# Kernel tuning notes

Hardware: AMD Instinct MI355X
Metric: run time of the kernel (lower is better)

The kernel has to match this reference:

```python
import jax, jax.numpy as jnp
import numpy as np

NEG_SLOPE = 0.1

def leaky(x):
    return jnp.where(x >= 0, x, NEG_SLOPE * x)

def setup_inputs() -> dict:
    key = jax.random.key(0)
    ks = jax.random.split(key, 9)
    B, N, K, Cin, Cout = 4, 16384, 16, 64, 128
    xyz = jax.random.normal(ks[0], (B, 3, N), jnp.float32)
    features = jax.random.normal(ks[1], (B, Cin, N), jnp.float32)
    knn_indices = jax.random.randint(ks[2], (B, N, K), 0, N)
    # weight_net: MLP2d(3, [8,16]) == two 1x1 convs with leaky_relu
    w1 = jax.random.normal(ks[3], (8, 3), jnp.float32) * 0.3
    b1 = jax.random.normal(ks[4], (8,), jnp.float32) * 0.05
    w2 = jax.random.normal(ks[5], (16, 8), jnp.float32) * 0.2
    b2 = jax.random.normal(ks[6], (16,), jnp.float32) * 0.05
    lin_w = jax.random.normal(ks[7], (Cout, 16 * (Cin + 3)), jnp.float32) * 0.02
    lin_b = jax.random.normal(ks[8], (Cout,), jnp.float32) * 0.02
    return {"xyz": xyz, "features": features, "knn_indices": knn_indices,
            "w1": w1, "b1": b1, "w2": w2, "b2": b2,
            "lin_w": lin_w, "lin_b": lin_b}

def reference(xyz, features, knn_indices, w1, b1, w2, b2, lin_w, lin_b):
    B, _, N = xyz.shape
    K = knn_indices.shape[2]
    # channel-last views
    xyz_cl = xyz.transpose(0, 2, 1)                                  # [B,N,3]
    feats_cl = jnp.concatenate([xyz, features], axis=1).transpose(0, 2, 1)  # [B,N,3+C]
    gather = jax.vmap(lambda f, i: f[i])                             # per-batch gather
    knn_xyz = gather(xyz_cl, knn_indices)                            # [B,N,K,3]
    knn_xyz_norm = knn_xyz - xyz_cl[:, :, None, :]                   # [B,N,K,3]
    # weight_net (1x1 conv MLP: 3 -> 8 -> 16, leaky_relu)
    h = leaky(jnp.einsum('bnkc,oc->bnko', knn_xyz_norm, w1) + b1)    # [B,N,K,8]
    w = leaky(jnp.einsum('bnkh,oh->bnko', h, w2) + b2)               # [B,N,K,16]
    knn_feats = gather(feats_cl, knn_indices)                        # [B,N,K,3+C]
    # weights^T @ knn_features, flattened (16, 3+C) -> 16*(3+C)
    agg = jnp.einsum('bnkw,bnkc->bnwc', w, knn_feats).reshape(B, N, -1)
    out = leaky(agg @ lin_w.T + lin_b)                               # [B,N,Cout]
    return out.transpose(0, 2, 1)                                    # [B,Cout,N]
```

## Files before the change

### kernel.cpp

```cpp
#include <hip/hip_runtime.h>
#include <hip/hip_bf16.h>

#define B_    4
#define N_    16384
#define K_    16
#define CIN_  64
#define CF_   67
#define COUT_ 128
#define AGGP_ 1088
#define P_    32
#define PH_   16
#define FSTR  64
#define ASTR  1096
#define WTS   272
#define NEG_  0.1f

typedef __attribute__((ext_vector_type(8))) short short8;
typedef __attribute__((ext_vector_type(4))) float f32x4;
typedef __attribute__((ext_vector_type(2))) unsigned int uint2_t;
typedef __attribute__((ext_vector_type(4))) unsigned int uint4_t;

__device__ __forceinline__ unsigned short f2b(float f) {
    __hip_bfloat16 h = __float2bfloat16(f);
    return *reinterpret_cast<unsigned short*>(&h);
}
__device__ __forceinline__ float leaky(float x) { return x >= 0.f ? x : NEG_ * x; }

__global__ __launch_bounds__(256) void pc_prep(
    const float* __restrict__ xyz,
    const float* __restrict__ feats,
    const float* __restrict__ lin_w,
    unsigned short* __restrict__ ft,
    short* __restrict__ lwb,
    float* __restrict__ xyz3)
{
    const int bid = blockIdx.x, t = threadIdx.x;
    if (bid < 1024) {
        __shared__ float st[64][69];
        const int b  = bid >> 8;
        const int j0 = (bid & 255) << 6;
        for (int ii = t; ii < 68 * 16; ii += 256) {
            const int c = ii >> 4, jq = ii & 15;
            f32x4 v = {0.f, 0.f, 0.f, 0.f};
            if (c < 3)
                v = *(const f32x4*)(xyz   + ((size_t)b * 3    + c)       * N_ + j0 + 4 * jq);
            else if (c < CF_)
                v = *(const f32x4*)(feats + ((size_t)b * CIN_ + (c - 3)) * N_ + j0 + 4 * jq);
            st[4 * jq + 0][c] = v.x;
            st[4 * jq + 1][c] = v.y;
            st[4 * jq + 2][c] = v.z;
            st[4 * jq + 3][c] = v.w;
        }
        __syncthreads();
        if (t < 64) {
            f32x4 v = { st[t][0], st[t][1], st[t][2], 0.f };
            *(f32x4*)(xyz3 + ((size_t)(b * N_ + j0 + t)) * 4) = v;
        }
        uint4_t* outp4 = (uint4_t*)(ft + (size_t)(b * N_ + j0) * FSTR);
        for (int idx = t; idx < 64 * 8; idx += 256) {
            const int j2 = idx >> 3, q = idx & 7;
            const int cb = 3 + q * 8;
            unsigned u[4];
#pragma unroll
            for (int e = 0; e < 4; e++) {
                const int c0 = cb + 2 * e;
                u[e] = (unsigned)f2b(st[j2][c0]) | ((unsigned)f2b(st[j2][c0 + 1]) << 16);
            }
            uint4_t uu = { u[0], u[1], u[2], u[3] };
            outp4[idx] = uu;
        }
    } else {
        const int o = bid - 1024;
        const float* src = lin_w + (size_t)o * (16 * CF_);
        short*       dst = lwb   + (size_t)o * AGGP_;
        for (int i = t; i < AGGP_; i += 256) {
            const int w = i / 68, c = i % 68;
            const int sc = (c < 64) ? (3 + c) : (c - 64);
            dst[i] = (c < CF_) ? (short)f2b(src[w * CF_ + sc]) : (short)0;
        }
    }
}

__device__ __forceinline__ void gather_ft(const unsigned short* ftb, const int* ip,
                                          int s, uint2_t* fb)
{
#pragma unroll
    for (int k = 0; k < K_; k++) {
        const unsigned short* rec = ftb + (size_t)ip[k] * FSTR;
        fb[k] = *(const uint2_t*)(rec + 4 * s);
    }
}

__device__ __forceinline__ void mlp_store(
    short* wd, float d0, float d1, float d2,
    const float* w1, const float* b1, const float* w2, const float* b2)
{
    float hh[8];
#pragma unroll
    for (int i = 0; i < 8; i++)
        hh[i] = leaky(b1[i] + w1[i*3+0]*d0 + w1[i*3+1]*d1 + w1[i*3+2]*d2);
#pragma unroll
    for (int w = 0; w < 16; w++) {
        float a = b2[w];
#pragma unroll
        for (int i = 0; i < 8; i++) a += w2[w*8+i] * hh[i];
        wd[w * 16] = (short)f2b(leaky(a));
    }
}

__device__ __forceinline__ void transpose_store(
    short* frow, const uint2_t* fb, int s)
{
    const int hf = ((s >> 2) & 1) << 3;
#pragma unroll
    for (int i = 0; i < 4; i++) {
        const unsigned sel = (i & 1) ? 0x07060302u : 0x05040100u;
        unsigned pk[8];
#pragma unroll
        for (int d = 0; d < 8; d++) {
            const unsigned lo = (i < 2) ? fb[2*d].x   : fb[2*d].y;
            const unsigned hi = (i < 2) ? fb[2*d+1].x : fb[2*d+1].y;
            pk[d] = __builtin_amdgcn_perm(hi, lo, sel);
        }
        const int c   = 4 * s + i;
        const int row = c ^ (s & 3);
        uint4_t q0 = { pk[0], pk[1], pk[2], pk[3] };
        uint4_t q1 = { pk[4], pk[5], pk[6], pk[7] };
        *(uint4_t*)(frow + row * 16 + hf)       = q0;
        *(uint4_t*)(frow + row * 16 + (8 - hf)) = q1;
    }
    if (s == 3) {
        uint4_t z = {0u, 0u, 0u, 0u};
        *(uint4_t*)(frow + 67 * 16)     = z;
        *(uint4_t*)(frow + 67 * 16 + 8) = z;
    }
}

__device__ __forceinline__ void agg_mfma(short* s_aggp, const short* s_WTp,
                                         int t, int pbase)
{
    const int lane = t & 63;
    const int wq   = lane >> 4;
    const int pr   = lane & 15;
    const int pbl  = (t >> 6) * 4;
    const int kh   = (wq & 1) * 8;
    const int side = (wq < 2) ? 0 : 1;
    const int asid = (pr < 8) ? 0 : 1;
    const bool act = (side == asid);
    const int cq   = 4 * (wq & 1);
    const int c0   = pr & 7;
    const int bb   = c0 >> 2;
#pragma unroll
    for (int pair = 0; pair < 2; pair++) {
        const int lpA = pbl + 2 * pair;
        const int ppA = pbase + lpA;
        const short8 bfr = *(const short8*)(s_WTp + (lpA + side) * WTS + pr * 16 + kh);
        const short* ap  = s_aggp + (size_t)(ppA + asid) * ASTR;
        f32x4 D[9];
#pragma unroll
        for (int cc = 0; cc < 9; cc++) {
            const int row  = (c0 + 8 * cc) ^ ((bb + 2 * cc) & 3);
            const int khcc = kh ^ (((cc >> 1) & 1) << 3);
            short8 af = {0,0,0,0,0,0,0,0};
            if (act && (cc < 8 || c0 < 4))
                af = *(const short8*)(ap + row * 16 + khcc);
            D[cc] = __builtin_amdgcn_mfma_f32_16x16x32_bf16(
                        af, bfr, (f32x4){0.f,0.f,0.f,0.f}, 0, 0, 0);
        }
        __asm__ __volatile__("" ::: "memory");
        short* arow = s_aggp + (size_t)(ppA + side) * ASTR + pr * 68;
#pragma unroll
        for (int cc = 0; cc < 9; cc++) {
            if (cc == 8 && cq != 0) continue;
            const unsigned lo = (unsigned)f2b(D[cc].x) | ((unsigned)f2b(D[cc].y) << 16);
            const unsigned hi = (unsigned)f2b(D[cc].z) | ((unsigned)f2b(D[cc].w) << 16);
            uint2_t pk2 = { lo, hi };
            *(uint2_t*)(arow + 8 * cc + cq) = pk2;
        }
    }
}

__global__ __launch_bounds__(256, 2) void pc_main(
    const float*          __restrict__ x3,
    const unsigned short* __restrict__ ft,
    const int*            __restrict__ knn,
    const float* __restrict__ w1, const float* __restrict__ b1,
    const float* __restrict__ w2, const float* __restrict__ b2,
    const short* __restrict__ lwb, const float* __restrict__ lin_b,
    float* __restrict__ out)
{
    __shared__ __align__(16) short s_agg[P_ * ASTR];
    __shared__ __align__(16) short s_WT[PH_ * WTS];
    __shared__ int s_idx[2 * PH_ * K_];

    const int t   = threadIdx.x;
    const int bid = blockIdx.x;
    const int b   = bid >> 9;
    const int n0  = (bid & 511) << 5;
    const unsigned short* ftb = ft + (size_t)b * N_ * FSTR;
    const f32x4* x3b = (const f32x4*)x3 + (size_t)b * N_;

    const int p = t >> 4, s = t & 15;

    const int n_a = n0 + p, n_b = n0 + PH_ + p;
    const int ja = knn[((size_t)(b * N_ + n_a)) * K_ + s];
    const int jb = knn[((size_t)(b * N_ + n_b)) * K_ + s];
    s_idx[(0 * PH_ + p) * K_ + s] = ja;
    s_idx[(1 * PH_ + p) * K_ + s] = jb;
    const f32x4 qa = x3b[ja], qb = x3b[jb];
    const f32x4 ca = x3b[n_a], cb = x3b[n_b];
    const float dxa0 = qa.x - ca.x, dxa1 = qa.y - ca.y, dxa2 = qa.z - ca.z;
    const float dxb0 = qb.x - cb.x, dxb1 = qb.y - cb.y, dxb2 = qb.z - cb.z;
    __asm__ __volatile__("" ::: "memory");

    const int* ipa = s_idx + (0 * PH_ + p) * K_;
    const int* ipb = s_idx + (1 * PH_ + p) * K_;
    uint2_t fbA[K_], fbB[K_];
    gather_ft(ftb, ipa, s, fbA);
    gather_ft(ftb, ipb, s, fbB);

    {
        short* frow = s_agg + (size_t)p * ASTR;
        frow[64 * 16 + s] = (short)f2b(qa.x);
        frow[65 * 16 + s] = (short)f2b(qa.y);
        frow[66 * 16 + s] = (short)f2b(qa.z);
    }
    mlp_store(s_WT + p * WTS + s, dxa0, dxa1, dxa2, w1, b1, w2, b2);
    __asm__ __volatile__("" ::: "memory");
    transpose_store(s_agg + (size_t)p * ASTR, fbA, s);
    __asm__ __volatile__("" ::: "memory");
    agg_mfma(s_agg, s_WT, t, 0);
    __asm__ __volatile__("" ::: "memory");

    {
        short* frow = s_agg + (size_t)(PH_ + p) * ASTR;
        frow[64 * 16 + s] = (short)f2b(qb.x);
        frow[65 * 16 + s] = (short)f2b(qb.y);
        frow[66 * 16 + s] = (short)f2b(qb.z);
    }
    mlp_store(s_WT + p * WTS + s, dxb0, dxb1, dxb2, w1, b1, w2, b2);
    __asm__ __volatile__("" ::: "memory");
    transpose_store(s_agg + (size_t)(PH_ + p) * ASTR, fbB, s);
    __asm__ __volatile__("" ::: "memory");
    agg_mfma(s_agg, s_WT, t, PH_);

    {
        const int lane = t & 63, wid = t >> 6;
        const int quad = lane >> 4, pr = lane & 15;
        const int kq = quad * 8;
        const short* a0p = lwb + (size_t)(wid * 32 + pr) * AGGP_ + kq;
        const short* a1p = a0p + 16 * AGGP_;

        short8 pa0[6], pa1[6];
#pragma unroll
        for (int d = 0; d < 6; d++) {
            pa0[d] = *(const short8*)(a0p + 32 * d);
            pa1[d] = *(const short8*)(a1p + 32 * d);
        }
        __syncthreads();

        const short* bp0 = s_agg + (size_t)pr * ASTR + kq;
        const short* bp1 = s_agg + (size_t)(16 + pr) * ASTR + kq;
        f32x4 acc00 = {0.f, 0.f, 0.f, 0.f};
        f32x4 acc01 = {0.f, 0.f, 0.f, 0.f};
        f32x4 acc10 = {0.f, 0.f, 0.f, 0.f};
        f32x4 acc11 = {0.f, 0.f, 0.f, 0.f};

#pragma unroll
        for (int ks = 0; ks < 34; ks++) {
            const int d = ks % 6;
            const short8 a0c = pa0[d], a1c = pa1[d];
            if (ks + 6 < 34) {
                pa0[d] = *(const short8*)(a0p + 32 * (ks + 6));
                pa1[d] = *(const short8*)(a1p + 32 * (ks + 6));
            }
            const short8 b0 = *(const short8*)(bp0 + 32 * ks);
            const short8 b1 = *(const short8*)(bp1 + 32 * ks);
            acc00 = __builtin_amdgcn_mfma_f32_16x16x32_bf16(a0c, b0, acc00, 0, 0, 0);
            acc01 = __builtin_amdgcn_mfma_f32_16x16x32_bf16(a0c, b1, acc01, 0, 0, 0);
            acc10 = __builtin_amdgcn_mfma_f32_16x16x32_bf16(a1c, b0, acc10, 0, 0, 0);
            acc11 = __builtin_amdgcn_mfma_f32_16x16x32_bf16(a1c, b1, acc11, 0, 0, 0);
        }
        const int o0 = wid * 32 + quad * 4;
#pragma unroll
        for (int r = 0; r < 4; r++) {
            const int oA = o0 + r;
            const int oB = oA + 16;
            const float bA = lin_b[oA], bB = lin_b[oB];
            float* rowA = out + ((size_t)(b * COUT_ + oA)) * N_ + n0;
            float* rowB = out + ((size_t)(b * COUT_ + oB)) * N_ + n0;
            rowA[pr]      = leaky(acc00[r] + bA);
            rowA[16 + pr] = leaky(acc01[r] + bA);
            rowB[pr]      = leaky(acc10[r] + bB);
            rowB[16 + pr] = leaky(acc11[r] + bB);
        }
    }
}

extern "C" void kernel_launch(void* const* d_in, const int* in_sizes, int n_in,
                              void* d_out, int out_size, void* d_ws, size_t ws_size,
                              hipStream_t stream)
{
    const float* xyz   = (const float*)d_in[0];
    const float* feats = (const float*)d_in[1];
    const int*   knn   = (const int*)d_in[2];
    const float* w1    = (const float*)d_in[3];
    const float* b1    = (const float*)d_in[4];
    const float* w2    = (const float*)d_in[5];
    const float* b2    = (const float*)d_in[6];
    const float* lin_w = (const float*)d_in[7];
    const float* lin_b = (const float*)d_in[8];
    float* out = (float*)d_out;

    const size_t ftBytes  = (size_t)B_ * N_ * FSTR * sizeof(short);
    const size_t lwbBytes = (size_t)COUT_ * AGGP_ * sizeof(short);
    unsigned short* ft   = (unsigned short*)d_ws;
    short*          lwb  = (short*)((char*)d_ws + ftBytes);
    float*          xyz3 = (float*)((char*)d_ws + ftBytes + lwbBytes);

    hipLaunchKernelGGL(pc_prep, dim3(1024 + COUT_), dim3(256), 0, stream,
                       xyz, feats, lin_w, ft, lwb, xyz3);
    hipLaunchKernelGGL(pc_main, dim3(B_ * (N_ / P_)), dim3(256), 0, stream,
                       xyz3, ft, knn, w1, b1, w2, b2, lwb, lin_b, out);
}
```

Measured before the change: 183.3 us.

## Double threads per block to split gather, MLP, and output GEMM work

```diff
diff --git a/kernel.cpp b/kernel.cpp
--- a/kernel.cpp
+++ b/kernel.cpp
@@ -82,17 +82,17 @@
 }
 
 __device__ __forceinline__ void gather_ft(const unsigned short* ftb, const int* ip,
-                                          int s, uint2_t* fb)
+                                          int s5, unsigned* fb)
 {
 #pragma unroll
     for (int k = 0; k < K_; k++) {
         const unsigned short* rec = ftb + (size_t)ip[k] * FSTR;
-        fb[k] = *(const uint2_t*)(rec + 4 * s);
+        fb[k] = *(const unsigned*)(rec + 2 * s5);
     }
 }
 
 __device__ __forceinline__ void mlp_store(
-    short* wd, float d0, float d1, float d2,
+    short* wd, int wh, float d0, float d1, float d2,
     const float* w1, const float* b1, const float* w2, const float* b2)
 {
     float hh[8];
@@ -100,7 +100,8 @@
     for (int i = 0; i < 8; i++)
         hh[i] = leaky(b1[i] + w1[i*3+0]*d0 + w1[i*3+1]*d1 + w1[i*3+2]*d2);
 #pragma unroll
-    for (int w = 0; w < 16; w++) {
+    for (int j = 0; j < 8; j++) {
+        const int w = wh * 8 + j;
         float a = b2[w];
 #pragma unroll
         for (int i = 0; i < 8; i++) a += w2[w*8+i] * hh[i];
@@ -109,27 +110,24 @@
 }
 
 __device__ __forceinline__ void transpose_store(
-    short* frow, const uint2_t* fb, int s)
-{
-    const int hf = ((s >> 2) & 1) << 3;
-#pragma unroll
-    for (int i = 0; i < 4; i++) {
+    short* frow, const unsigned* fb, int s5)
+{
+#pragma unroll
+    for (int i = 0; i < 2; i++) {
         const unsigned sel = (i & 1) ? 0x07060302u : 0x05040100u;
         unsigned pk[8];
 #pragma unroll
-        for (int d = 0; d < 8; d++) {
-            const unsigned lo = (i < 2) ? fb[2*d].x   : fb[2*d].y;
-            const unsigned hi = (i < 2) ? fb[2*d+1].x : fb[2*d+1].y;
-            pk[d] = __builtin_amdgcn_perm(hi, lo, sel);
-        }
-        const int c   = 4 * s + i;
-        const int row = c ^ (s & 3);
+        for (int d = 0; d < 8; d++)
+            pk[d] = __builtin_amdgcn_perm(fb[2*d+1], fb[2*d], sel);
+        const int c   = 2 * s5 + i;
+        const int row = c ^ ((c >> 2) & 3);
+        const int hf  = ((c >> 4) & 1) << 3;
         uint4_t q0 = { pk[0], pk[1], pk[2], pk[3] };
         uint4_t q1 = { pk[4], pk[5], pk[6], pk[7] };
         *(uint4_t*)(frow + row * 16 + hf)       = q0;
         *(uint4_t*)(frow + row * 16 + (8 - hf)) = q1;
     }
-    if (s == 3) {
+    if (s5 == 3) {
         uint4_t z = {0u, 0u, 0u, 0u};
         *(uint4_t*)(frow + 67 * 16)     = z;
         *(uint4_t*)(frow + 67 * 16 + 8) = z;
@@ -142,7 +140,7 @@
     const int lane = t & 63;
     const int wq   = lane >> 4;
     const int pr   = lane & 15;
-    const int pbl  = (t >> 6) * 4;
+    const int pbl  = (t >> 6) * 2;
     const int kh   = (wq & 1) * 8;
     const int side = (wq < 2) ? 0 : 1;
     const int asid = (pr < 8) ? 0 : 1;
@@ -150,37 +148,33 @@
     const int cq   = 4 * (wq & 1);
     const int c0   = pr & 7;
     const int bb   = c0 >> 2;
-#pragma unroll
-    for (int pair = 0; pair < 2; pair++) {
-        const int lpA = pbl + 2 * pair;
-        const int ppA = pbase + lpA;
-        const short8 bfr = *(const short8*)(s_WTp + (lpA + side) * WTS + pr * 16 + kh);
-        const short* ap  = s_aggp + (size_t)(ppA + asid) * ASTR;
-        f32x4 D[9];
-#pragma unroll
-        for (int cc = 0; cc < 9; cc++) {
-            const int row  = (c0 + 8 * cc) ^ ((bb + 2 * cc) & 3);
-            const int khcc = kh ^ (((cc >> 1) & 1) << 3);
-            short8 af = {0,0,0,0,0,0,0,0};
-            if (act && (cc < 8 || c0 < 4))
-                af = *(const short8*)(ap + row * 16 + khcc);
-            D[cc] = __builtin_amdgcn_mfma_f32_16x16x32_bf16(
-                        af, bfr, (f32x4){0.f,0.f,0.f,0.f}, 0, 0, 0);
-        }
-        __asm__ __volatile__("" ::: "memory");
-        short* arow = s_aggp + (size_t)(ppA + side) * ASTR + pr * 68;
-#pragma unroll
-        for (int cc = 0; cc < 9; cc++) {
-            if (cc == 8 && cq != 0) continue;
-            const unsigned lo = (unsigned)f2b(D[cc].x) | ((unsigned)f2b(D[cc].y) << 16);
-            const unsigned hi = (unsigned)f2b(D[cc].z) | ((unsigned)f2b(D[cc].w) << 16);
-            uint2_t pk2 = { lo, hi };
-            *(uint2_t*)(arow + 8 * cc + cq) = pk2;
-        }
-    }
-}
-
-__global__ __launch_bounds__(256, 2) void pc_main(
+    const int ppA  = pbase + pbl;
+    const short8 bfr = *(const short8*)(s_WTp + (pbl + side) * WTS + pr * 16 + kh);
+    const short* ap  = s_aggp + (size_t)(ppA + asid) * ASTR;
+    f32x4 D[9];
+#pragma unroll
+    for (int cc = 0; cc < 9; cc++) {
+        const int row  = (c0 + 8 * cc) ^ ((bb + 2 * cc) & 3);
+        const int khcc = kh ^ (((cc >> 1) & 1) << 3);
+        short8 af = {0,0,0,0,0,0,0,0};
+        if (act && (cc < 8 || c0 < 4))
+            af = *(const short8*)(ap + row * 16 + khcc);
+        D[cc] = __builtin_amdgcn_mfma_f32_16x16x32_bf16(
+                    af, bfr, (f32x4){0.f,0.f,0.f,0.f}, 0, 0, 0);
+    }
+    __asm__ __volatile__("" ::: "memory");
+    short* arow = s_aggp + (size_t)(ppA + side) * ASTR + pr * 68;
+#pragma unroll
+    for (int cc = 0; cc < 9; cc++) {
+        if (cc == 8 && cq != 0) continue;
+        const unsigned lo = (unsigned)f2b(D[cc].x) | ((unsigned)f2b(D[cc].y) << 16);
+        const unsigned hi = (unsigned)f2b(D[cc].z) | ((unsigned)f2b(D[cc].w) << 16);
+        uint2_t pk2 = { lo, hi };
+        *(uint2_t*)(arow + 8 * cc + cq) = pk2;
+    }
+}
+
+__global__ __launch_bounds__(512, 4) void pc_main(
     const float*          __restrict__ x3,
     const unsigned short* __restrict__ ft,
     const int*            __restrict__ knn,
@@ -200,13 +194,18 @@
     const unsigned short* ftb = ft + (size_t)b * N_ * FSTR;
     const f32x4* x3b = (const f32x4*)x3 + (size_t)b * N_;
 
-    const int p = t >> 4, s = t & 15;
+    const int p  = t >> 5;
+    const int s5 = t & 31;
+    const int k  = s5 & 15;
+    const int wh = s5 >> 4;
 
     const int n_a = n0 + p, n_b = n0 + PH_ + p;
-    const int ja = knn[((size_t)(b * N_ + n_a)) * K_ + s];
-    const int jb = knn[((size_t)(b * N_ + n_b)) * K_ + s];
-    s_idx[(0 * PH_ + p) * K_ + s] = ja;
-    s_idx[(1 * PH_ + p) * K_ + s] = jb;
+    const int ja = knn[((size_t)(b * N_ + n_a)) * K_ + k];
+    const int jb = knn[((size_t)(b * N_ + n_b)) * K_ + k];
+    if (wh == 0) {
+        s_idx[(0 * PH_ + p) * K_ + k] = ja;
+        s_idx[(1 * PH_ + p) * K_ + k] = jb;
+    }
     const f32x4 qa = x3b[ja], qb = x3b[jb];
     const f32x4 ca = x3b[n_a], cb = x3b[n_b];
     const float dxa0 = qa.x - ca.x, dxa1 = qa.y - ca.y, dxa2 = qa.z - ca.z;
@@ -215,32 +214,32 @@
 
     const int* ipa = s_idx + (0 * PH_ + p) * K_;
     const int* ipb = s_idx + (1 * PH_ + p) * K_;
-    uint2_t fbA[K_], fbB[K_];
-    gather_ft(ftb, ipa, s, fbA);
-    gather_ft(ftb, ipb, s, fbB);
-
-    {
+    unsigned fbA[K_], fbB[K_];
+    gather_ft(ftb, ipa, s5, fbA);
+    gather_ft(ftb, ipb, s5, fbB);
+
+    if (wh == 0) {
         short* frow = s_agg + (size_t)p * ASTR;
-        frow[64 * 16 + s] = (short)f2b(qa.x);
-        frow[65 * 16 + s] = (short)f2b(qa.y);
-        frow[66 * 16 + s] = (short)f2b(qa.z);
-    }
-    mlp_store(s_WT + p * WTS + s, dxa0, dxa1, dxa2, w1, b1, w2, b2);
-    __asm__ __volatile__("" ::: "memory");
-    transpose_store(s_agg + (size_t)p * ASTR, fbA, s);
+        frow[64 * 16 + k] = (short)f2b(qa.x);
+        frow[65 * 16 + k] = (short)f2b(qa.y);
+        frow[66 * 16 + k] = (short)f2b(qa.z);
+    }
+    mlp_store(s_WT + p * WTS + k, wh, dxa0, dxa1, dxa2, w1, b1, w2, b2);
+    __asm__ __volatile__("" ::: "memory");
+    transpose_store(s_agg + (size_t)p * ASTR, fbA, s5);
     __asm__ __volatile__("" ::: "memory");
     agg_mfma(s_agg, s_WT, t, 0);
     __asm__ __volatile__("" ::: "memory");
 
-    {
+    if (wh == 0) {
         short* frow = s_agg + (size_t)(PH_ + p) * ASTR;
-        frow[64 * 16 + s] = (short)f2b(qb.x);
-        frow[65 * 16 + s] = (short)f2b(qb.y);
-        frow[66 * 16 + s] = (short)f2b(qb.z);
-    }
-    mlp_store(s_WT + p * WTS + s, dxb0, dxb1, dxb2, w1, b1, w2, b2);
-    __asm__ __volatile__("" ::: "memory");
-    transpose_store(s_agg + (size_t)(PH_ + p) * ASTR, fbB, s);
+        frow[64 * 16 + k] = (short)f2b(qb.x);
+        frow[65 * 16 + k] = (short)f2b(qb.y);
+        frow[66 * 16 + k] = (short)f2b(qb.z);
+    }
+    mlp_store(s_WT + p * WTS + k, wh, dxb0, dxb1, dxb2, w1, b1, w2, b2);
+    __asm__ __volatile__("" ::: "memory");
+    transpose_store(s_agg + (size_t)(PH_ + p) * ASTR, fbB, s5);
     __asm__ __volatile__("" ::: "memory");
     agg_mfma(s_agg, s_WT, t, PH_);
 
@@ -248,51 +247,38 @@
         const int lane = t & 63, wid = t >> 6;
         const int quad = lane >> 4, pr = lane & 15;
         const int kq = quad * 8;
-        const short* a0p = lwb + (size_t)(wid * 32 + pr) * AGGP_ + kq;
-        const short* a1p = a0p + 16 * AGGP_;
-
-        short8 pa0[6], pa1[6];
-#pragma unroll
-        for (int d = 0; d < 6; d++) {
+        const short* a0p = lwb + (size_t)(wid * 16 + pr) * AGGP_ + kq;
+
+        short8 pa0[6];
+#pragma unroll
+        for (int d = 0; d < 6; d++)
             pa0[d] = *(const short8*)(a0p + 32 * d);
-            pa1[d] = *(const short8*)(a1p + 32 * d);
-        }
         __syncthreads();
 
         const short* bp0 = s_agg + (size_t)pr * ASTR + kq;
         const short* bp1 = s_agg + (size_t)(16 + pr) * ASTR + kq;
         f32x4 acc00 = {0.f, 0.f, 0.f, 0.f};
         f32x4 acc01 = {0.f, 0.f, 0.f, 0.f};
-        f32x4 acc10 = {0.f, 0.f, 0.f, 0.f};
-        f32x4 acc11 = {0.f, 0.f, 0.f, 0.f};
 
 #pragma unroll
         for (int ks = 0; ks < 34; ks++) {
             const int d = ks % 6;
-            const short8 a0c = pa0[d], a1c = pa1[d];
-            if (ks + 6 < 34) {
+            const short8 a0c = pa0[d];
+            if (ks + 6 < 34)
                 pa0[d] = *(const short8*)(a0p + 32 * (ks + 6));
-                pa1[d] = *(const short8*)(a1p + 32 * (ks + 6));
-            }
             const short8 b0 = *(const short8*)(bp0 + 32 * ks);
             const short8 b1 = *(const short8*)(bp1 + 32 * ks);
             acc00 = __builtin_amdgcn_mfma_f32_16x16x32_bf16(a0c, b0, acc00, 0, 0, 0);
             acc01 = __builtin_amdgcn_mfma_f32_16x16x32_bf16(a0c, b1, acc01, 0, 0, 0);
-            acc10 = __builtin_amdgcn_mfma_f32_16x16x32_bf16(a1c, b0, acc10, 0, 0, 0);
-            acc11 = __builtin_amdgcn_mfma_f32_16x16x32_bf16(a1c, b1, acc11, 0, 0, 0);
-        }
-        const int o0 = wid * 32 + quad * 4;
+        }
+        const int o0 = wid * 16 + quad * 4;
 #pragma unroll
         for (int r = 0; r < 4; r++) {
             const int oA = o0 + r;
-            const int oB = oA + 16;
-            const float bA = lin_b[oA], bB = lin_b[oB];
+            const float bA = lin_b[oA];
             float* rowA = out + ((size_t)(b * COUT_ + oA)) * N_ + n0;
-            float* rowB = out + ((size_t)(b * COUT_ + oB)) * N_ + n0;
             rowA[pr]      = leaky(acc00[r] + bA);
             rowA[16 + pr] = leaky(acc01[r] + bA);
-            rowB[pr]      = leaky(acc10[r] + bB);
-            rowB[16 + pr] = leaky(acc11[r] + bB);
         }
     }
 }
@@ -320,6 +306,6 @@
 
     hipLaunchKernelGGL(pc_prep, dim3(1024 + COUT_), dim3(256), 0, stream,
                        xyz, feats, lin_w, ft, lwb, xyz3);
-    hipLaunchKernelGGL(pc_main, dim3(B_ * (N_ / P_)), dim3(256), 0, stream,
+    hipLaunchKernelGGL(pc_main, dim3(B_ * (N_ / P_)), dim3(512), 0, stream,
                        xyz3, ft, knn, w1, b1, w2, b2, lwb, lin_b, out);
 }
```

After: 202.7 us. 10.6% more time.

## Halve points per block to 16 and raise occupancy to three blocks per CU

Applied to the files above, without the earlier changes.

```diff
diff --git a/kernel.cpp b/kernel.cpp
--- a/kernel.cpp
+++ b/kernel.cpp
@@ -8,8 +8,7 @@
 #define CF_   67
 #define COUT_ 128
 #define AGGP_ 1088
-#define P_    32
-#define PH_   16
+#define P_    16
 #define FSTR  64
 #define ASTR  1096
 #define WTS   272
@@ -136,8 +135,7 @@
     }
 }
 
-__device__ __forceinline__ void agg_mfma(short* s_aggp, const short* s_WTp,
-                                         int t, int pbase)
+__device__ __forceinline__ void agg_mfma(short* s_aggp, const short* s_WTp, int t)
 {
     const int lane = t & 63;
     const int wq   = lane >> 4;
@@ -152,10 +150,9 @@
     const int bb   = c0 >> 2;
 #pragma unroll
     for (int pair = 0; pair < 2; pair++) {
-        const int lpA = pbl + 2 * pair;
-        const int ppA = pbase + lpA;
-        const short8 bfr = *(const short8*)(s_WTp + (lpA + side) * WTS + pr * 16 + kh);
-        const short* ap  = s_aggp + (size_t)(ppA + asid) * ASTR;
+        const int pA = pbl + 2 * pair;
+        const short8 bfr = *(const short8*)(s_WTp + (pA + side) * WTS + pr * 16 + kh);
+        const short* ap  = s_aggp + (size_t)(pA + asid) * ASTR;
         f32x4 D[9];
 #pragma unroll
         for (int cc = 0; cc < 9; cc++) {
@@ -168,7 +165,7 @@
                         af, bfr, (f32x4){0.f,0.f,0.f,0.f}, 0, 0, 0);
         }
         __asm__ __volatile__("" ::: "memory");
-        short* arow = s_aggp + (size_t)(ppA + side) * ASTR + pr * 68;
+        short* arow = s_aggp + (size_t)(pA + side) * ASTR + pr * 68;
 #pragma unroll
         for (int cc = 0; cc < 9; cc++) {
             if (cc == 8 && cq != 0) continue;
@@ -180,7 +177,7 @@
     }
 }
 
-__global__ __launch_bounds__(256, 2) void pc_main(
+__global__ __launch_bounds__(256, 3) void pc_main(
     const float*          __restrict__ x3,
     const unsigned short* __restrict__ ft,
     const int*            __restrict__ knn,
@@ -190,34 +187,29 @@
     float* __restrict__ out)
 {
     __shared__ __align__(16) short s_agg[P_ * ASTR];
-    __shared__ __align__(16) short s_WT[PH_ * WTS];
-    __shared__ int s_idx[2 * PH_ * K_];
+    __shared__ __align__(16) short s_WT[P_ * WTS];
+    __shared__ int s_idx[P_ * K_];
 
     const int t   = threadIdx.x;
     const int bid = blockIdx.x;
-    const int b   = bid >> 9;
-    const int n0  = (bid & 511) << 5;
+    const int b   = bid >> 10;
+    const int n0  = (bid & 1023) << 4;
     const unsigned short* ftb = ft + (size_t)b * N_ * FSTR;
     const f32x4* x3b = (const f32x4*)x3 + (size_t)b * N_;
 
     const int p = t >> 4, s = t & 15;
 
-    const int n_a = n0 + p, n_b = n0 + PH_ + p;
+    const int n_a = n0 + p;
     const int ja = knn[((size_t)(b * N_ + n_a)) * K_ + s];
-    const int jb = knn[((size_t)(b * N_ + n_b)) * K_ + s];
-    s_idx[(0 * PH_ + p) * K_ + s] = ja;
-    s_idx[(1 * PH_ + p) * K_ + s] = jb;
-    const f32x4 qa = x3b[ja], qb = x3b[jb];
-    const f32x4 ca = x3b[n_a], cb = x3b[n_b];
+    s_idx[p * K_ + s] = ja;
+    const f32x4 qa = x3b[ja];
+    const f32x4 ca = x3b[n_a];
     const float dxa0 = qa.x - ca.x, dxa1 = qa.y - ca.y, dxa2 = qa.z - ca.z;
-    const float dxb0 = qb.x - cb.x, dxb1 = qb.y - cb.y, dxb2 = qb.z - cb.z;
     __asm__ __volatile__("" ::: "memory");
 
-    const int* ipa = s_idx + (0 * PH_ + p) * K_;
-    const int* ipb = s_idx + (1 * PH_ + p) * K_;
-    uint2_t fbA[K_], fbB[K_];
+    const int* ipa = s_idx + p * K_;
+    uint2_t fbA[K_];
     gather_ft(ftb, ipa, s, fbA);
-    gather_ft(ftb, ipb, s, fbB);
 
     {
         short* frow = s_agg + (size_t)p * ASTR;
@@ -229,20 +221,7 @@
     __asm__ __volatile__("" ::: "memory");
     transpose_store(s_agg + (size_t)p * ASTR, fbA, s);
     __asm__ __volatile__("" ::: "memory");
-    agg_mfma(s_agg, s_WT, t, 0);
-    __asm__ __volatile__("" ::: "memory");
-
-    {
-        short* frow = s_agg + (size_t)(PH_ + p) * ASTR;
-        frow[64 * 16 + s] = (short)f2b(qb.x);
-        frow[65 * 16 + s] = (short)f2b(qb.y);
-        frow[66 * 16 + s] = (short)f2b(qb.z);
-    }
-    mlp_store(s_WT + p * WTS + s, dxb0, dxb1, dxb2, w1, b1, w2, b2);
-    __asm__ __volatile__("" ::: "memory");
-    transpose_store(s_agg + (size_t)(PH_ + p) * ASTR, fbB, s);
-    __asm__ __volatile__("" ::: "memory");
-    agg_mfma(s_agg, s_WT, t, PH_);
+    agg_mfma(s_agg, s_WT, t);
 
     {
         const int lane = t & 63, wid = t >> 6;
@@ -259,12 +238,9 @@
         }
         __syncthreads();
 
-        const short* bp0 = s_agg + (size_t)pr * ASTR + kq;
-        const short* bp1 = s_agg + (size_t)(16 + pr) * ASTR + kq;
-        f32x4 acc00 = {0.f, 0.f, 0.f, 0.f};
-        f32x4 acc01 = {0.f, 0.f, 0.f, 0.f};
-        f32x4 acc10 = {0.f, 0.f, 0.f, 0.f};
-        f32x4 acc11 = {0.f, 0.f, 0.f, 0.f};
+        const short* bp = s_agg + (size_t)pr * ASTR + kq;
+        f32x4 acc0 = {0.f, 0.f, 0.f, 0.f};
+        f32x4 acc1 = {0.f, 0.f, 0.f, 0.f};
 
 #pragma unroll
         for (int ks = 0; ks < 34; ks++) {
@@ -274,25 +250,19 @@
                 pa0[d] = *(const short8*)(a0p + 32 * (ks + 6));
                 pa1[d] = *(const short8*)(a1p + 32 * (ks + 6));
             }
-            const short8 b0 = *(const short8*)(bp0 + 32 * ks);
-            const short8 b1 = *(const short8*)(bp1 + 32 * ks);
-            acc00 = __builtin_amdgcn_mfma_f32_16x16x32_bf16(a0c, b0, acc00, 0, 0, 0);
-            acc01 = __builtin_amdgcn_mfma_f32_16x16x32_bf16(a0c, b1, acc01, 0, 0, 0);
-            acc10 = __builtin_amdgcn_mfma_f32_16x16x32_bf16(a1c, b0, acc10, 0, 0, 0);
-            acc11 = __builtin_amdgcn_mfma_f32_16x16x32_bf16(a1c, b1, acc11, 0, 0, 0);
+            const short8 bfr = *(const short8*)(bp + 32 * ks);
+            acc0 = __builtin_amdgcn_mfma_f32_16x16x32_bf16(a0c, bfr, acc0, 0, 0, 0);
+            acc1 = __builtin_amdgcn_mfma_f32_16x16x32_bf16(a1c, bfr, acc1, 0, 0, 0);
         }
         const int o0 = wid * 32 + quad * 4;
 #pragma unroll
         for (int r = 0; r < 4; r++) {
             const int oA = o0 + r;
             const int oB = oA + 16;
-            const float bA = lin_b[oA], bB = lin_b[oB];
-            float* rowA = out + ((size_t)(b * COUT_ + oA)) * N_ + n0;
-            float* rowB = out + ((size_t)(b * COUT_ + oB)) * N_ + n0;
-            rowA[pr]      = leaky(acc00[r] + bA);
-            rowA[16 + pr] = leaky(acc01[r] + bA);
-            rowB[pr]      = leaky(acc10[r] + bB);
-            rowB[16 + pr] = leaky(acc11[r] + bB);
+            const float vA = leaky(acc0[r] + lin_b[oA]);
+            const float vB = leaky(acc1[r] + lin_b[oB]);
+            out[((size_t)(b * COUT_ + oA)) * N_ + n0 + pr] = vA;
+            out[((size_t)(b * COUT_ + oB)) * N_ + n0 + pr] = vB;
         }
     }
 }
```

Result: slower. 226.8 us (+23.7%).
